# Optimization experiments

Hardware: AMD Instinct MI355X
Metric: run time of the kernel (lower is better)

## Reference

```python
import jax, jax.numpy as jnp
import numpy as np

N_NODES = 100000
N_EDGES = 1600000
IN_C, HID, N_CLS = 128, 128, 40


def setup_inputs() -> dict:
    key = jax.random.key(0)
    ks = jax.random.split(key, 8)
    x = jax.random.normal(ks[0], (N_NODES, IN_C), dtype=jnp.float32)
    edge_index = jax.random.randint(ks[1], (2, N_EDGES), 0, N_NODES, dtype=jnp.int64)
    s1 = 1.0 / np.sqrt(IN_C)
    s2 = 1.0 / np.sqrt(HID)
    return {
        "x": x,
        "edge_index": edge_index,
        "Wl1": jax.random.normal(ks[2], (IN_C, HID), dtype=jnp.float32) * s1,
        "Wr1": jax.random.normal(ks[3], (IN_C, HID), dtype=jnp.float32) * s1,
        "b1": jnp.zeros((HID,), dtype=jnp.float32),
        "Wl2": jax.random.normal(ks[4], (HID, N_CLS), dtype=jnp.float32) * s2,
        "Wr2": jax.random.normal(ks[5], (HID, N_CLS), dtype=jnp.float32) * s2,
        "b2": jnp.zeros((N_CLS,), dtype=jnp.float32),
    }


def _sage_conv(x, src, dst, Wl, Wr, b):
    # mean-aggregate neighbor features at destination nodes
    n = x.shape[0]
    agg = jax.ops.segment_sum(x[src], dst, num_segments=n)           # [N, C]
    cnt = jax.ops.segment_sum(jnp.ones((src.shape[0],), x.dtype), dst, num_segments=n)
    mean = agg / jnp.maximum(cnt, 1.0)[:, None]
    return mean @ Wl + x @ Wr + b


def reference(x, edge_index, Wl1, Wr1, b1, Wl2, Wr2, b2):
    src, dst = edge_index[0], edge_index[1]
    h = jax.nn.relu(_sage_conv(x, src, dst, Wl1, Wr1, b1))
    return _sage_conv(h, src, dst, Wl2, Wr2, b2)
```

## Files before the change

kernel.cpp:

```cpp
#include <hip/hip_runtime.h>

#define C_IN 128
#define N_CLS 40
#define ZB   40

#define NPB   256
#define MAXNB 512
#define CAP   6144
#define BCSTR 16
#define BINB  8192

typedef __attribute__((ext_vector_type(8))) short bf16x8;
typedef __attribute__((ext_vector_type(4))) float f32x4;
typedef __attribute__((ext_vector_type(2))) float f32x2;

__device__ __forceinline__ ushort f2b(float f) {
  union { float f; unsigned u; } v; v.f = f;
  unsigned r = v.u + 0x7FFF + ((v.u >> 16) & 1);
  return (ushort)(r >> 16);
}
__device__ __forceinline__ unsigned packbf(float lo, float hi) {
  return (unsigned)f2b(lo) | ((unsigned)f2b(hi) << 16);
}
__device__ __forceinline__ void acc2(float& fa, float& fb, unsigned u) {
  union { unsigned u; float f; } lo, hi;
  lo.u = u << 16; hi.u = u & 0xFFFF0000u;
  fa += lo.f; fb += hi.f;
}

#if __has_builtin(__builtin_amdgcn_cvt_pk_f32_fp8) && __has_builtin(__builtin_amdgcn_cvt_pk_fp8_f32)
#define HW_FP8 1
#else
#define HW_FP8 0
#endif

__device__ __forceinline__ float f8dec1(unsigned b) {
  unsigned E = (b >> 3) & 15, M = b & 7;
  if (E) {
    union { unsigned u; float f; } v;
    v.u = ((b & 0x80u) << 24) | ((E + 120u) << 23) | (M << 20);
    return v.f;
  }
  float m = (float)(int)M * 0.001953125f;
  return (b & 0x80u) ? -m : m;
}
__device__ __forceinline__ unsigned f8enc1(float x) {
  union { float f; unsigned u; } v; v.f = x;
  unsigned s = (v.u >> 31) << 7;
  float ax = fabsf(x);
  if (ax < 9.765625e-4f) return s;
  if (ax < 0.015625f) {
    int M = (int)rintf(ax * 512.0f);
    return (M >= 8) ? (s | 0x08u) : (s | (unsigned)M);
  }
  if (ax > 448.0f) return s | 0x7Eu;
  unsigned au = v.u & 0x7FFFFFFFu;
  unsigned r = au + 0x7FFFFu + ((au >> 20) & 1);
  int e = (int)(r >> 23) - 127;
  unsigned M = (r >> 20) & 7;
  if (e > 8) return s | 0x7Eu;
  return s | ((unsigned)(e + 7) << 3) | M;
}
__device__ __forceinline__ void accf8x4(float* a, unsigned u) {
#if HW_FP8
  f32x2 lo = __builtin_amdgcn_cvt_pk_f32_fp8((int)u, false);
  f32x2 hi = __builtin_amdgcn_cvt_pk_f32_fp8((int)u, true);
  a[0] += lo[0]; a[1] += lo[1]; a[2] += hi[0]; a[3] += hi[1];
#else
  a[0] += f8dec1(u & 0xFF); a[1] += f8dec1((u >> 8) & 0xFF);
  a[2] += f8dec1((u >> 16) & 0xFF); a[3] += f8dec1(u >> 24);
#endif
}
__device__ __forceinline__ unsigned packf8x4(float x0, float x1, float x2, float x3) {
#if HW_FP8
  int p = 0;
  p = __builtin_amdgcn_cvt_pk_fp8_f32(x0, x1, p, false);
  p = __builtin_amdgcn_cvt_pk_fp8_f32(x2, x3, p, true);
  return (unsigned)p;
#else
  return f8enc1(x0) | (f8enc1(x1) << 8) | (f8enc1(x2) << 16) | (f8enc1(x3) << 24);
#endif
}
__device__ __forceinline__ unsigned char f8enc_byte(float x) {
#if HW_FP8
  return (unsigned char)(__builtin_amdgcn_cvt_pk_fp8_f32(x, x, 0, false) & 0xFF);
#else
  return (unsigned char)f8enc1(x);
#endif
}

__global__ __launch_bounds__(256) void bin_cvt_kernel(
    const int* __restrict__ src, const int* __restrict__ dst,
    int* __restrict__ bcur, unsigned* __restrict__ staged, int E, int NB, int nbin,
    const float* __restrict__ xin, ushort* __restrict__ xb,
    unsigned char* __restrict__ xf8, long n8)
{
  __shared__ unsigned sw[BINB];
  __shared__ ushort  sb[BINB];
  __shared__ int cnt[MAXNB];
  __shared__ int base[MAXNB];
  const int tid = threadIdx.x;
  if (blockIdx.x >= nbin) {
    long i = ((long)(blockIdx.x - nbin) * 256 + tid);
    if (i < n8) {
      const float4 a = *reinterpret_cast<const float4*>(xin + i * 8);
      const float4 b = *reinterpret_cast<const float4*>(xin + i * 8 + 4);
      uint4 o;
      o.x = packbf(a.x, a.y);
      o.y = packbf(a.z, a.w);
      o.z = packbf(b.x, b.y);
      o.w = packbf(b.z, b.w);
      *reinterpret_cast<uint4*>(xb + i * 8) = o;
      uint2 p;
      p.x = packf8x4(a.x, a.y, a.z, a.w);
      p.y = packf8x4(b.x, b.y, b.z, b.w);
      *reinterpret_cast<uint2*>(xf8 + i * 8) = p;
    }
    return;
  }
  for (int i = tid; i < NB; i += 256) cnt[i] = 0;
  __syncthreads();
  const int e0 = blockIdx.x * BINB;
  const int nE = min(BINB, E - e0);
  for (int k = tid; k < nE; k += 256) {
    int d = dst[e0 + k];
    int s = src[e0 + k];
    int b = d >> 8;
    sw[k] = (unsigned)s | ((unsigned)(d & 255) << 20);
    sb[k] = (ushort)b;
    atomicAdd(&cnt[b], 1);
  }
  __syncthreads();
  for (int i = tid; i < NB; i += 256) {
    int c = cnt[i];
    base[i] = (c > 0) ? atomicAdd(&bcur[i * BCSTR], c) : 0;
    cnt[i] = 0;
  }
  __syncthreads();
  for (int k = tid; k < nE; k += 256) {
    int b = sb[k];
    int pos = base[b] + atomicAdd(&cnt[b], 1);
    if (pos < CAP)
      staged[(size_t)b * CAP + pos] = sw[k];
  }
}

__global__ __launch_bounds__(256) void csr_kernel(
    const unsigned* __restrict__ staged, const int* __restrict__ bcur,
    int* __restrict__ row_ptr, int* __restrict__ deg, int* __restrict__ csr_src, int N)
{
  __shared__ unsigned st[CAP];
  __shared__ int dcnt[NPB];
  __shared__ int cur[NPB];
  __shared__ int wsum[4];
  __shared__ int rb_s;
  const int b = blockIdx.x, tid = threadIdx.x;
  const int cb = min(bcur[b * BCSTR], CAP);
  for (int i = tid; i < cb; i += 256) st[i] = staged[(size_t)b * CAP + i];
  int part = 0;
  for (int i = tid; i < b; i += 256) part += min(bcur[i * BCSTR], CAP);
  if (tid == 0) rb_s = 0;
  dcnt[tid] = 0;
  __syncthreads();
  #pragma unroll
  for (int off = 32; off > 0; off >>= 1) part += __shfl_down(part, off);
  if ((tid & 63) == 0 && part != 0) atomicAdd(&rb_s, part);
  for (int i = tid; i < cb; i += 256) atomicAdd(&dcnt[st[i] >> 20], 1);
  __syncthreads();
  const int rb = rb_s;
  int d = dcnt[tid];
  const int lane = tid & 63, w = tid >> 6;
  int inc = d;
  #pragma unroll
  for (int off = 1; off < 64; off <<= 1) {
    int v = __shfl_up(inc, off);
    if (lane >= off) inc += v;
  }
  if (lane == 63) wsum[w] = inc;
  __syncthreads();
  int wo = 0;
  for (int i = 0; i < w; ++i) wo += wsum[i];
  const int excl = wo + inc - d;
  cur[tid] = excl;
  const int node = b * NPB + tid;
  if (node < N) { row_ptr[node] = rb + excl; deg[node] = d; }
  __syncthreads();
  for (int i = tid; i < cb; i += 256) {
    unsigned wv = st[i];
    int p = atomicAdd(&cur[wv >> 20], 1);
    csr_src[rb + p] = (int)(wv & 0xFFFFF);
  }
}

__global__ __launch_bounds__(256) void agg1_kernel(
    const unsigned char* __restrict__ xf8, const ushort* __restrict__ xb,
    const int* __restrict__ csr_src, const int* __restrict__ row_ptr,
    const int* __restrict__ deg, ushort* __restrict__ mean, int N)
{
  int t = blockIdx.x * 256 + threadIdx.x;
  int n = t >> 3;
  if (n >= N) return;
  int q = t & 7;
  int base = row_ptr[n];
  int d = deg[n];
  float a[16];
  #pragma unroll
  for (int i = 0; i < 16; ++i) a[i] = 0.f;
  if (d > 8) {
    const unsigned char* fq = xf8 + q * 16;
    int j = 0;
    for (; j + 4 <= d; j += 4) {
      int s0 = csr_src[base + j + 0];
      int s1 = csr_src[base + j + 1];
      int s2 = csr_src[base + j + 2];
      int s3 = csr_src[base + j + 3];
      uint4 v0 = *reinterpret_cast<const uint4*>(fq + (size_t)s0 * C_IN);
      uint4 v1 = *reinterpret_cast<const uint4*>(fq + (size_t)s1 * C_IN);
      uint4 v2 = *reinterpret_cast<const uint4*>(fq + (size_t)s2 * C_IN);
      uint4 v3 = *reinterpret_cast<const uint4*>(fq + (size_t)s3 * C_IN);
      accf8x4(a+0, v0.x); accf8x4(a+4, v0.y); accf8x4(a+8, v0.z); accf8x4(a+12, v0.w);
      accf8x4(a+0, v1.x); accf8x4(a+4, v1.y); accf8x4(a+8, v1.z); accf8x4(a+12, v1.w);
      accf8x4(a+0, v2.x); accf8x4(a+4, v2.y); accf8x4(a+8, v2.z); accf8x4(a+12, v2.w);
      accf8x4(a+0, v3.x); accf8x4(a+4, v3.y); accf8x4(a+8, v3.z); accf8x4(a+12, v3.w);
    }
    for (; j < d; ++j) {
      int s = csr_src[base + j];
      uint4 v = *reinterpret_cast<const uint4*>(fq + (size_t)s * C_IN);
      accf8x4(a+0, v.x); accf8x4(a+4, v.y); accf8x4(a+8, v.z); accf8x4(a+12, v.w);
    }
  } else {
    const ushort* fq = xb + q * 16;
    for (int j = 0; j < d; ++j) {
      int s = csr_src[base + j];
      uint4 w0 = *reinterpret_cast<const uint4*>(fq + (size_t)s * C_IN);
      uint4 w1 = *reinterpret_cast<const uint4*>(fq + (size_t)s * C_IN + 8);
      acc2(a[0],a[1],w0.x); acc2(a[2],a[3],w0.y); acc2(a[4],a[5],w0.z); acc2(a[6],a[7],w0.w);
      acc2(a[8],a[9],w1.x); acc2(a[10],a[11],w1.y); acc2(a[12],a[13],w1.z); acc2(a[14],a[15],w1.w);
    }
  }
  float inv = (d > 0) ? (1.0f / (float)d) : 0.0f;
  uint4 o0, o1;
  o0.x = packbf(a[0]*inv, a[1]*inv);  o0.y = packbf(a[2]*inv, a[3]*inv);
  o0.z = packbf(a[4]*inv, a[5]*inv);  o0.w = packbf(a[6]*inv, a[7]*inv);
  o1.x = packbf(a[8]*inv, a[9]*inv);  o1.y = packbf(a[10]*inv, a[11]*inv);
  o1.z = packbf(a[12]*inv, a[13]*inv); o1.w = packbf(a[14]*inv, a[15]*inv);
  uint4* mp = reinterpret_cast<uint4*>(mean + (size_t)n * C_IN + q * 16);
  mp[0] = o0;
  mp[1] = o1;
}

__global__ __launch_bounds__(256) void layer1_mfma(
    const ushort* __restrict__ xb, const ushort* __restrict__ mb,
    const float* __restrict__ Wr, const float* __restrict__ Wl,
    const float* __restrict__ bias, ushort* __restrict__ h, int N, int ntiles)
{
  __shared__ ushort sB[8 * 8 * 64 * 8];
  const int tid = threadIdx.x;
  for (int idx = tid; idx < 8 * 8 * 64; idx += 256) {
    int l  = idx & 63;
    int cg = (idx >> 6) & 7;
    int ks = idx >> 9;
    int c  = cg * 16 + (l & 15);
    int kb = ks * 32 + 8 * (l >> 4);
    ushort* p = &sB[idx * 8];
    #pragma unroll
    for (int j = 0; j < 8; ++j) {
      int k = kb + j;
      float w = (k < C_IN) ? Wr[k * C_IN + c] : Wl[(k - C_IN) * C_IN + c];
      p[j] = f2b(w);
    }
  }
  __syncthreads();
  const int w = tid >> 6, l = tid & 63;
  const int rfrag = l & 15, kg = l >> 4;
  for (int tile = blockIdx.x; tile < ntiles; tile += gridDim.x) {
    int n0 = tile * 128 + w * 32;
    int rc0 = n0 + rfrag;      rc0 = (rc0 < N) ? rc0 : (N - 1);
    int rc1 = n0 + 16 + rfrag; rc1 = (rc1 < N) ? rc1 : (N - 1);
    f32x4 acc[2][8] = {};
    #pragma unroll
    for (int ks = 0; ks < 8; ++ks) {
      int kb = ks * 32 + kg * 8;
      const ushort* Asrc = (kb < C_IN) ? (xb + kb) : (mb + (kb - C_IN));
      bf16x8 a0 = *reinterpret_cast<const bf16x8*>(Asrc + (size_t)rc0 * C_IN);
      bf16x8 a1 = *reinterpret_cast<const bf16x8*>(Asrc + (size_t)rc1 * C_IN);
      #pragma unroll
      for (int cg = 0; cg < 8; ++cg) {
        bf16x8 b = *reinterpret_cast<const bf16x8*>(&sB[((ks * 8 + cg) * 64 + l) * 8]);
        acc[0][cg] = __builtin_amdgcn_mfma_f32_16x16x32_bf16(a0, b, acc[0][cg], 0, 0, 0);
        acc[1][cg] = __builtin_amdgcn_mfma_f32_16x16x32_bf16(a1, b, acc[1][cg], 0, 0, 0);
      }
    }
    const int rowoff = (l >> 4) * 4, colbase = l & 15;
    #pragma unroll
    for (int f = 0; f < 2; ++f) {
      #pragma unroll
      for (int cg = 0; cg < 8; ++cg) {
        int c = cg * 16 + colbase;
        float bc = bias[c];
        #pragma unroll
        for (int r = 0; r < 4; ++r) {
          int row = n0 + f * 16 + rowoff + r;
          if (row < N) {
            float v = fmaxf(acc[f][cg][r] + bc, 0.0f);
            h[(size_t)row * C_IN + c] = f2b(v);
          }
        }
      }
    }
  }
}

__global__ __launch_bounds__(256) void gemm2_dual(
    const ushort* __restrict__ hb,
    const float* __restrict__ Wl, const float* __restrict__ Wr,
    unsigned char* __restrict__ z, float* __restrict__ out, int N, int ntiles)
{
  __shared__ ushort sBl[4 * 3 * 64 * 8];
  __shared__ ushort sBr[4 * 3 * 64 * 8];
  const int tid = threadIdx.x;
  for (int idx = tid; idx < 4 * 3 * 64; idx += 256) {
    int l  = idx & 63;
    int cg = (idx >> 6) % 3;
    int ks = idx / (3 * 64);
    int c  = cg * 16 + (l & 15);
    int kb = ks * 32 + 8 * (l >> 4);
    ushort* pl = &sBl[idx * 8];
    ushort* pr = &sBr[idx * 8];
    #pragma unroll
    for (int j = 0; j < 8; ++j) {
      int k = kb + j;
      float wl = 0.0f, wr = 0.0f;
      if (c < N_CLS) { wl = Wl[k * N_CLS + c]; wr = Wr[k * N_CLS + c]; }
      pl[j] = f2b(wl);
      pr[j] = f2b(wr);
    }
  }
  __syncthreads();
  const int w = tid >> 6, l = tid & 63;
  const int rfrag = l & 15, kg = l >> 4;
  for (int tile = blockIdx.x; tile < ntiles; tile += gridDim.x) {
    int n0 = tile * 128 + w * 32;
    int rc0 = n0 + rfrag;      rc0 = (rc0 < N) ? rc0 : (N - 1);
    int rc1 = n0 + 16 + rfrag; rc1 = (rc1 < N) ? rc1 : (N - 1);
    f32x4 az[2][3] = {};
    f32x4 ay[2][3] = {};
    #pragma unroll
    for (int ks = 0; ks < 4; ++ks) {
      int kb = ks * 32 + kg * 8;
      bf16x8 a0 = *reinterpret_cast<const bf16x8*>(hb + (size_t)rc0 * C_IN + kb);
      bf16x8 a1 = *reinterpret_cast<const bf16x8*>(hb + (size_t)rc1 * C_IN + kb);
      #pragma unroll
      for (int cg = 0; cg < 3; ++cg) {
        bf16x8 bl = *reinterpret_cast<const bf16x8*>(&sBl[((ks * 3 + cg) * 64 + l) * 8]);
        bf16x8 br = *reinterpret_cast<const bf16x8*>(&sBr[((ks * 3 + cg) * 64 + l) * 8]);
        az[0][cg] = __builtin_amdgcn_mfma_f32_16x16x32_bf16(a0, bl, az[0][cg], 0, 0, 0);
        az[1][cg] = __builtin_amdgcn_mfma_f32_16x16x32_bf16(a1, bl, az[1][cg], 0, 0, 0);
        ay[0][cg] = __builtin_amdgcn_mfma_f32_16x16x32_bf16(a0, br, ay[0][cg], 0, 0, 0);
        ay[1][cg] = __builtin_amdgcn_mfma_f32_16x16x32_bf16(a1, br, ay[1][cg], 0, 0, 0);
      }
    }
    const int rowoff = (l >> 4) * 4, colbase = l & 15;
    #pragma unroll
    for (int f = 0; f < 2; ++f) {
      #pragma unroll
      for (int cg = 0; cg < 3; ++cg) {
        int c = cg * 16 + colbase;
        if (c < N_CLS) {
          #pragma unroll
          for (int r = 0; r < 4; ++r) {
            int row = n0 + f * 16 + rowoff + r;
            if (row < N) {
              z[(size_t)row * ZB + c] = f8enc_byte(az[f][cg][r]);
              out[(size_t)row * N_CLS + c] = ay[f][cg][r];
            }
          }
        }
      }
    }
  }
}

__global__ __launch_bounds__(256) void agg2z_kernel(
    const unsigned char* __restrict__ z, const int* __restrict__ csr_src,
    const int* __restrict__ row_ptr, const int* __restrict__ deg,
    const float* __restrict__ b2, float* __restrict__ out, int N)
{
  unsigned w = blockIdx.x * 256 + threadIdx.x;
  unsigned n = w / 5u;
  if (n >= (unsigned)N) return;
  unsigned q = w - n * 5u;
  const unsigned char* zq = z + q * 8;
  int base = row_ptr[n];
  int d = deg[n];
  float a[8];
  #pragma unroll
  for (int i = 0; i < 8; ++i) a[i] = 0.f;
  int j = 0;
  for (; j + 4 <= d; j += 4) {
    int s0 = csr_src[base + j + 0];
    int s1 = csr_src[base + j + 1];
    int s2 = csr_src[base + j + 2];
    int s3 = csr_src[base + j + 3];
    uint2 v0 = *reinterpret_cast<const uint2*>(zq + (size_t)s0 * ZB);
    uint2 v1 = *reinterpret_cast<const uint2*>(zq + (size_t)s1 * ZB);
    uint2 v2 = *reinterpret_cast<const uint2*>(zq + (size_t)s2 * ZB);
    uint2 v3 = *reinterpret_cast<const uint2*>(zq + (size_t)s3 * ZB);
    accf8x4(a+0, v0.x); accf8x4(a+4, v0.y);
    accf8x4(a+0, v1.x); accf8x4(a+4, v1.y);
    accf8x4(a+0, v2.x); accf8x4(a+4, v2.y);
    accf8x4(a+0, v3.x); accf8x4(a+4, v3.y);
  }
  for (; j < d; ++j) {
    int s = csr_src[base + j];
    uint2 v = *reinterpret_cast<const uint2*>(zq + (size_t)s * ZB);
    accf8x4(a+0, v.x); accf8x4(a+4, v.y);
  }
  float inv = (d > 0) ? (1.0f / (float)d) : 0.0f;
  float* op = out + (size_t)n * N_CLS + q * 8;
  const float4 bA = *reinterpret_cast<const float4*>(b2 + q * 8);
  const float4 bB = *reinterpret_cast<const float4*>(b2 + q * 8 + 4);
  float4 y0 = *reinterpret_cast<const float4*>(op);
  float4 y1 = *reinterpret_cast<const float4*>(op + 4);
  y0.x += a[0] * inv + bA.x; y0.y += a[1] * inv + bA.y;
  y0.z += a[2] * inv + bA.z; y0.w += a[3] * inv + bA.w;
  y1.x += a[4] * inv + bB.x; y1.y += a[5] * inv + bB.y;
  y1.z += a[6] * inv + bB.z; y1.w += a[7] * inv + bB.w;
  *reinterpret_cast<float4*>(op) = y0;
  *reinterpret_cast<float4*>(op + 4) = y1;
}

extern "C" void kernel_launch(void* const* d_in, const int* in_sizes, int n_in,
                              void* d_out, int out_size, void* d_ws, size_t ws_size,
                              hipStream_t stream)
{
  const float* x   = (const float*)d_in[0];
  const int*   ei  = (const int*)d_in[1];
  const float* Wl1 = (const float*)d_in[2];
  const float* Wr1 = (const float*)d_in[3];
  const float* b1  = (const float*)d_in[4];
  const float* Wl2 = (const float*)d_in[5];
  const float* Wr2 = (const float*)d_in[6];
  const float* b2  = (const float*)d_in[7];
  float* out = (float*)d_out;

  const int N = in_sizes[0] / C_IN;
  const int E = in_sizes[1] / 2;
  const int* src = ei;
  const int* dst = ei + E;
  const int NB = (N + NPB - 1) / NPB;

  size_t Np = ((size_t)N + 255) & ~(size_t)255;
  size_t Ep = ((size_t)E + 255) & ~(size_t)255;
  int* wsi     = (int*)d_ws;
  int* bcur    = wsi;
  int* row_ptr = wsi + (size_t)MAXNB * BCSTR;
  int* deg     = row_ptr + Np;
  int* csr_src = deg + Np;
  unsigned* staged = (unsigned*)(csr_src + Ep);
  unsigned char* zb = (unsigned char*)staged;
  ushort* xb    = (ushort*)(staged + (size_t)MAXNB * CAP);
  ushort* meanb = xb + (size_t)N * C_IN;
  ushort* hb    = meanb + (size_t)N * C_IN;
  unsigned char* xf8 = (unsigned char*)(hb + (size_t)N * C_IN);

  hipMemsetAsync(bcur, 0, (size_t)MAXNB * BCSTR * sizeof(int), stream);

  const int nbin = (E + BINB - 1) / BINB;
  long n8 = (long)N * C_IN / 8;
  const int ncvt = (int)((n8 + 255) / 256);
  bin_cvt_kernel<<<nbin + ncvt, 256, 0, stream>>>(src, dst, bcur, staged, E, NB, nbin,
                                                  x, xb, xf8, n8);

  csr_kernel<<<NB, 256, 0, stream>>>(staged, bcur, row_ptr, deg, csr_src, N);

  const int ntiles = (N + 127) / 128;

  agg1_kernel<<<(N * 8 + 255) / 256, 256, 0, stream>>>(xf8, xb, csr_src, row_ptr, deg, meanb, N);
  layer1_mfma<<<512, 256, 0, stream>>>(xb, meanb, Wr1, Wl1, b1, hb, N, ntiles);

  gemm2_dual<<<512, 256, 0, stream>>>(hb, Wl2, Wr2, zb, out, N, ntiles);
  agg2z_kernel<<<(N * 5 + 255) / 256, 256, 0, stream>>>(zb, csr_src, row_ptr, deg, b2, out, N);
}
```

Before: 170.8 us.

## Transform-then-aggregate layer 1 and fuse CSR build with dense GEMM

Layer 1 is reordered so x is first multiplied by Wr and Wl, giving u = x@Wr + b and v = x@Wl. Neighbours of v are then mean-aggregated, and relu is applied to the sum with u inside the aggregation kernel. The dense GEMM now runs in the same launch as the CSR build, in extra blocks, because it does not depend on the graph. This removes one kernel launch and the separate mean buffer pass, and lets the GEMM overlap with CSR construction. In exchange, v is written in both fp8 and bf16 with scalar per-element stores, the xb buffer is overwritten in place, and the union shared-memory layout at 512 threads may reduce occupancy.

Measured after the change: 203.9 us. 1.19x slower.

```diff
diff --git a/kernel.cpp b/kernel.cpp
--- a/kernel.cpp
+++ b/kernel.cpp
@@ -26,6 +26,11 @@
   union { unsigned u; float f; } lo, hi;
   lo.u = u << 16; hi.u = u & 0xFFFF0000u;
   fa += lo.f; fb += hi.f;
+}
+__device__ __forceinline__ unsigned relu2add(float m0, float m1, unsigned uu) {
+  union { unsigned u; float f; } lo, hi;
+  lo.u = uu << 16; hi.u = uu & 0xFFFF0000u;
+  return packbf(fmaxf(m0 + lo.f, 0.0f), fmaxf(m1 + hi.f, 0.0f));
 }
 
 #if __has_builtin(__builtin_amdgcn_cvt_pk_f32_fp8) && __has_builtin(__builtin_amdgcn_cvt_pk_fp8_f32)
@@ -71,16 +76,6 @@
   a[2] += f8dec1((u >> 16) & 0xFF); a[3] += f8dec1(u >> 24);
 #endif
 }
-__device__ __forceinline__ unsigned packf8x4(float x0, float x1, float x2, float x3) {
-#if HW_FP8
-  int p = 0;
-  p = __builtin_amdgcn_cvt_pk_fp8_f32(x0, x1, p, false);
-  p = __builtin_amdgcn_cvt_pk_fp8_f32(x2, x3, p, true);
-  return (unsigned)p;
-#else
-  return f8enc1(x0) | (f8enc1(x1) << 8) | (f8enc1(x2) << 16) | (f8enc1(x3) << 24);
-#endif
-}
 __device__ __forceinline__ unsigned char f8enc_byte(float x) {
 #if HW_FP8
   return (unsigned char)(__builtin_amdgcn_cvt_pk_fp8_f32(x, x, 0, false) & 0xFF);
@@ -92,8 +87,7 @@
 __global__ __launch_bounds__(256) void bin_cvt_kernel(
     const int* __restrict__ src, const int* __restrict__ dst,
     int* __restrict__ bcur, unsigned* __restrict__ staged, int E, int NB, int nbin,
-    const float* __restrict__ xin, ushort* __restrict__ xb,
-    unsigned char* __restrict__ xf8, long n8)
+    const float* __restrict__ xin, ushort* __restrict__ xb, long n8)
 {
   __shared__ unsigned sw[BINB];
   __shared__ ushort  sb[BINB];
@@ -111,10 +105,6 @@
       o.z = packbf(b.x, b.y);
       o.w = packbf(b.z, b.w);
       *reinterpret_cast<uint4*>(xb + i * 8) = o;
-      uint2 p;
-      p.x = packf8x4(a.x, a.y, a.z, a.w);
-      p.y = packf8x4(b.x, b.y, b.z, b.w);
-      *reinterpret_cast<uint2*>(xf8 + i * 8) = p;
     }
     return;
   }
@@ -145,57 +135,127 @@
   }
 }
 
-__global__ __launch_bounds__(256) void csr_kernel(
+union SharedCG {
+  struct { unsigned st[CAP]; int dcnt[NPB]; int cur[NPB]; int wsum[4]; int rb_s; } c;
+  struct { ushort bu[4 * 8 * 64 * 8]; ushort bv[4 * 8 * 64 * 8]; } g;
+};
+
+__global__ __launch_bounds__(512) void csr_gemm1_kernel(
     const unsigned* __restrict__ staged, const int* __restrict__ bcur,
-    int* __restrict__ row_ptr, int* __restrict__ deg, int* __restrict__ csr_src, int N)
-{
-  __shared__ unsigned st[CAP];
-  __shared__ int dcnt[NPB];
-  __shared__ int cur[NPB];
-  __shared__ int wsum[4];
-  __shared__ int rb_s;
-  const int b = blockIdx.x, tid = threadIdx.x;
-  const int cb = min(bcur[b * BCSTR], CAP);
-  for (int i = tid; i < cb; i += 256) st[i] = staged[(size_t)b * CAP + i];
-  int part = 0;
-  for (int i = tid; i < b; i += 256) part += min(bcur[i * BCSTR], CAP);
-  if (tid == 0) rb_s = 0;
-  dcnt[tid] = 0;
+    int* __restrict__ row_ptr, int* __restrict__ deg, int* __restrict__ csr_src,
+    int N, int NB, int ntiles, int ngem,
+    ushort* __restrict__ xb,
+    const float* __restrict__ Wr, const float* __restrict__ Wl,
+    const float* __restrict__ bias,
+    ushort* __restrict__ u, unsigned char* __restrict__ vf8)
+{
+  __shared__ SharedCG sh;
+  const int tid = threadIdx.x;
+  if (blockIdx.x < NB) {
+    const int b = blockIdx.x;
+    const int cb = min(bcur[b * BCSTR], CAP);
+    for (int i = tid; i < cb; i += 512) sh.c.st[i] = staged[(size_t)b * CAP + i];
+    int part = 0;
+    for (int i = tid; i < b; i += 512) part += min(bcur[i * BCSTR], CAP);
+    if (tid == 0) sh.c.rb_s = 0;
+    if (tid < 256) sh.c.dcnt[tid] = 0;
+    __syncthreads();
+    #pragma unroll
+    for (int off = 32; off > 0; off >>= 1) part += __shfl_down(part, off);
+    if ((tid & 63) == 0 && part != 0) atomicAdd(&sh.c.rb_s, part);
+    for (int i = tid; i < cb; i += 512) atomicAdd(&sh.c.dcnt[sh.c.st[i] >> 20], 1);
+    __syncthreads();
+    const int rb = sh.c.rb_s;
+    int d = 0, excl = 0;
+    if (tid < 256) {
+      d = sh.c.dcnt[tid];
+      const int lane = tid & 63, w = tid >> 6;
+      int inc = d;
+      #pragma unroll
+      for (int off = 1; off < 64; off <<= 1) {
+        int v = __shfl_up(inc, off);
+        if (lane >= off) inc += v;
+      }
+      if (lane == 63) sh.c.wsum[w] = inc;
+      excl = inc - d;
+    }
+    __syncthreads();
+    if (tid < 256) {
+      int wo = 0;
+      for (int i = 0; i < (tid >> 6); ++i) wo += sh.c.wsum[i];
+      excl += wo;
+      sh.c.cur[tid] = excl;
+      const int node = b * NPB + tid;
+      if (node < N) { row_ptr[node] = rb + excl; deg[node] = d; }
+    }
+    __syncthreads();
+    for (int i = tid; i < cb; i += 512) {
+      unsigned wv = sh.c.st[i];
+      int p = atomicAdd(&sh.c.cur[wv >> 20], 1);
+      csr_src[rb + p] = (int)(wv & 0xFFFFF);
+    }
+    return;
+  }
+  for (int idx = tid; idx < 4 * 8 * 64; idx += 512) {
+    int l  = idx & 63;
+    int cg = (idx >> 6) & 7;
+    int ks = idx >> 9;
+    int c  = cg * 16 + (l & 15);
+    int kb = ks * 32 + 8 * (l >> 4);
+    ushort* pu = &sh.g.bu[idx * 8];
+    ushort* pv = &sh.g.bv[idx * 8];
+    #pragma unroll
+    for (int j = 0; j < 8; ++j) {
+      int k = kb + j;
+      pu[j] = f2b(Wr[k * C_IN + c]);
+      pv[j] = f2b(Wl[k * C_IN + c]);
+    }
+  }
   __syncthreads();
-  #pragma unroll
-  for (int off = 32; off > 0; off >>= 1) part += __shfl_down(part, off);
-  if ((tid & 63) == 0 && part != 0) atomicAdd(&rb_s, part);
-  for (int i = tid; i < cb; i += 256) atomicAdd(&dcnt[st[i] >> 20], 1);
-  __syncthreads();
-  const int rb = rb_s;
-  int d = dcnt[tid];
-  const int lane = tid & 63, w = tid >> 6;
-  int inc = d;
-  #pragma unroll
-  for (int off = 1; off < 64; off <<= 1) {
-    int v = __shfl_up(inc, off);
-    if (lane >= off) inc += v;
-  }
-  if (lane == 63) wsum[w] = inc;
-  __syncthreads();
-  int wo = 0;
-  for (int i = 0; i < w; ++i) wo += wsum[i];
-  const int excl = wo + inc - d;
-  cur[tid] = excl;
-  const int node = b * NPB + tid;
-  if (node < N) { row_ptr[node] = rb + excl; deg[node] = d; }
-  __syncthreads();
-  for (int i = tid; i < cb; i += 256) {
-    unsigned wv = st[i];
-    int p = atomicAdd(&cur[wv >> 20], 1);
-    csr_src[rb + p] = (int)(wv & 0xFFFFF);
-  }
-}
-
-__global__ __launch_bounds__(256) void agg1_kernel(
-    const unsigned char* __restrict__ xf8, const ushort* __restrict__ xb,
-    const int* __restrict__ csr_src, const int* __restrict__ row_ptr,
-    const int* __restrict__ deg, ushort* __restrict__ mean, int N)
+  const int wv = tid >> 6, l = tid & 63;
+  const int kg = l >> 4;
+  for (int tile = blockIdx.x - NB; tile < ntiles; tile += ngem) {
+    const int n0 = tile * 128 + wv * 16;
+    int rc = n0 + (l & 15); rc = (rc < N) ? rc : (N - 1);
+    f32x4 au[8] = {};
+    f32x4 av[8] = {};
+    #pragma unroll
+    for (int ks = 0; ks < 4; ++ks) {
+      int kb = ks * 32 + kg * 8;
+      bf16x8 a = *reinterpret_cast<const bf16x8*>(xb + (size_t)rc * C_IN + kb);
+      #pragma unroll
+      for (int cg = 0; cg < 8; ++cg) {
+        bf16x8 bu = *reinterpret_cast<const bf16x8*>(&sh.g.bu[((ks * 8 + cg) * 64 + l) * 8]);
+        bf16x8 bv = *reinterpret_cast<const bf16x8*>(&sh.g.bv[((ks * 8 + cg) * 64 + l) * 8]);
+        au[cg] = __builtin_amdgcn_mfma_f32_16x16x32_bf16(a, bu, au[cg], 0, 0, 0);
+        av[cg] = __builtin_amdgcn_mfma_f32_16x16x32_bf16(a, bv, av[cg], 0, 0, 0);
+      }
+    }
+    const int rowoff = (l >> 4) * 4, colbase = l & 15;
+    #pragma unroll
+    for (int cg = 0; cg < 8; ++cg) {
+      int c = cg * 16 + colbase;
+      float bc = bias[c];
+      #pragma unroll
+      for (int r = 0; r < 4; ++r) {
+        int row = n0 + rowoff + r;
+        if (row < N) {
+          float uu = au[cg][r] + bc;
+          float vvv = av[cg][r];
+          u[(size_t)row * C_IN + c] = f2b(uu);
+          vf8[(size_t)row * C_IN + c] = f8enc_byte(vvv);
+          xb[(size_t)row * C_IN + c] = f2b(vvv);
+        }
+      }
+    }
+  }
+}
+
+__global__ __launch_bounds__(256) void agg1v_kernel(
+    const unsigned char* __restrict__ vf8, const ushort* __restrict__ vb,
+    const ushort* __restrict__ u, const int* __restrict__ csr_src,
+    const int* __restrict__ row_ptr, const int* __restrict__ deg,
+    ushort* __restrict__ h, int N)
 {
   int t = blockIdx.x * 256 + threadIdx.x;
   int n = t >> 3;
@@ -207,7 +267,7 @@
   #pragma unroll
   for (int i = 0; i < 16; ++i) a[i] = 0.f;
   if (d > 8) {
-    const unsigned char* fq = xf8 + q * 16;
+    const unsigned char* fq = vf8 + q * 16;
     int j = 0;
     for (; j + 4 <= d; j += 4) {
       int s0 = csr_src[base + j + 0];
@@ -229,7 +289,7 @@
       accf8x4(a+0, v.x); accf8x4(a+4, v.y); accf8x4(a+8, v.z); accf8x4(a+12, v.w);
     }
   } else {
-    const ushort* fq = xb + q * 16;
+    const ushort* fq = vb + q * 16;
     for (int j = 0; j < d; ++j) {
       int s = csr_src[base + j];
       uint4 w0 = *reinterpret_cast<const uint4*>(fq + (size_t)s * C_IN);
@@ -239,76 +299,21 @@
     }
   }
   float inv = (d > 0) ? (1.0f / (float)d) : 0.0f;
+  const ushort* up = u + (size_t)n * C_IN + q * 16;
+  uint4 u0 = *reinterpret_cast<const uint4*>(up);
+  uint4 u1 = *reinterpret_cast<const uint4*>(up + 8);
   uint4 o0, o1;
-  o0.x = packbf(a[0]*inv, a[1]*inv);  o0.y = packbf(a[2]*inv, a[3]*inv);
-  o0.z = packbf(a[4]*inv, a[5]*inv);  o0.w = packbf(a[6]*inv, a[7]*inv);
-  o1.x = packbf(a[8]*inv, a[9]*inv);  o1.y = packbf(a[10]*inv, a[11]*inv);
-  o1.z = packbf(a[12]*inv, a[13]*inv); o1.w = packbf(a[14]*inv, a[15]*inv);
-  uint4* mp = reinterpret_cast<uint4*>(mean + (size_t)n * C_IN + q * 16);
-  mp[0] = o0;
-  mp[1] = o1;
-}
-
-__global__ __launch_bounds__(256) void layer1_mfma(
-    const ushort* __restrict__ xb, const ushort* __restrict__ mb,
-    const float* __restrict__ Wr, const float* __restrict__ Wl,
-    const float* __restrict__ bias, ushort* __restrict__ h, int N, int ntiles)
-{
-  __shared__ ushort sB[8 * 8 * 64 * 8];
-  const int tid = threadIdx.x;
-  for (int idx = tid; idx < 8 * 8 * 64; idx += 256) {
-    int l  = idx & 63;
-    int cg = (idx >> 6) & 7;
-    int ks = idx >> 9;
-    int c  = cg * 16 + (l & 15);
-    int kb = ks * 32 + 8 * (l >> 4);
-    ushort* p = &sB[idx * 8];
-    #pragma unroll
-    for (int j = 0; j < 8; ++j) {
-      int k = kb + j;
-      float w = (k < C_IN) ? Wr[k * C_IN + c] : Wl[(k - C_IN) * C_IN + c];
-      p[j] = f2b(w);
-    }
-  }
-  __syncthreads();
-  const int w = tid >> 6, l = tid & 63;
-  const int rfrag = l & 15, kg = l >> 4;
-  for (int tile = blockIdx.x; tile < ntiles; tile += gridDim.x) {
-    int n0 = tile * 128 + w * 32;
-    int rc0 = n0 + rfrag;      rc0 = (rc0 < N) ? rc0 : (N - 1);
-    int rc1 = n0 + 16 + rfrag; rc1 = (rc1 < N) ? rc1 : (N - 1);
-    f32x4 acc[2][8] = {};
-    #pragma unroll
-    for (int ks = 0; ks < 8; ++ks) {
-      int kb = ks * 32 + kg * 8;
-      const ushort* Asrc = (kb < C_IN) ? (xb + kb) : (mb + (kb - C_IN));
-      bf16x8 a0 = *reinterpret_cast<const bf16x8*>(Asrc + (size_t)rc0 * C_IN);
-      bf16x8 a1 = *reinterpret_cast<const bf16x8*>(Asrc + (size_t)rc1 * C_IN);
-      #pragma unroll
-      for (int cg = 0; cg < 8; ++cg) {
-        bf16x8 b = *reinterpret_cast<const bf16x8*>(&sB[((ks * 8 + cg) * 64 + l) * 8]);
-        acc[0][cg] = __builtin_amdgcn_mfma_f32_16x16x32_bf16(a0, b, acc[0][cg], 0, 0, 0);
-        acc[1][cg] = __builtin_amdgcn_mfma_f32_16x16x32_bf16(a1, b, acc[1][cg], 0, 0, 0);
-      }
-    }
-    const int rowoff = (l >> 4) * 4, colbase = l & 15;
-    #pragma unroll
-    for (int f = 0; f < 2; ++f) {
-      #pragma unroll
-      for (int cg = 0; cg < 8; ++cg) {
-        int c = cg * 16 + colbase;
-        float bc = bias[c];
-        #pragma unroll
-        for (int r = 0; r < 4; ++r) {
-          int row = n0 + f * 16 + rowoff + r;
-          if (row < N) {
-            float v = fmaxf(acc[f][cg][r] + bc, 0.0f);
-            h[(size_t)row * C_IN + c] = f2b(v);
-          }
-        }
-      }
-    }
-  }
+  o0.x = relu2add(a[0]*inv,  a[1]*inv,  u0.x);
+  o0.y = relu2add(a[2]*inv,  a[3]*inv,  u0.y);
+  o0.z = relu2add(a[4]*inv,  a[5]*inv,  u0.z);
+  o0.w = relu2add(a[6]*inv,  a[7]*inv,  u0.w);
+  o1.x = relu2add(a[8]*inv,  a[9]*inv,  u1.x);
+  o1.y = relu2add(a[10]*inv, a[11]*inv, u1.y);
+  o1.z = relu2add(a[12]*inv, a[13]*inv, u1.z);
+  o1.w = relu2add(a[14]*inv, a[15]*inv, u1.w);
+  uint4* hp = reinterpret_cast<uint4*>(h + (size_t)n * C_IN + q * 16);
+  hp[0] = o0;
+  hp[1] = o1;
 }
 
 __global__ __launch_bounds__(256) void gemm2_dual(
@@ -460,9 +465,9 @@
   unsigned* staged = (unsigned*)(csr_src + Ep);
   unsigned char* zb = (unsigned char*)staged;
   ushort* xb    = (ushort*)(staged + (size_t)MAXNB * CAP);
-  ushort* meanb = xb + (size_t)N * C_IN;
-  ushort* hb    = meanb + (size_t)N * C_IN;
-  unsigned char* xf8 = (unsigned char*)(hb + (size_t)N * C_IN);
+  ushort* ub    = xb + (size_t)N * C_IN;
+  ushort* hb    = ub + (size_t)N * C_IN;
+  unsigned char* vf8 = (unsigned char*)(hb + (size_t)N * C_IN);
 
   hipMemsetAsync(bcur, 0, (size_t)MAXNB * BCSTR * sizeof(int), stream);
 
@@ -470,14 +475,16 @@
   long n8 = (long)N * C_IN / 8;
   const int ncvt = (int)((n8 + 255) / 256);
   bin_cvt_kernel<<<nbin + ncvt, 256, 0, stream>>>(src, dst, bcur, staged, E, NB, nbin,
-                                                  x, xb, xf8, n8);
-
-  csr_kernel<<<NB, 256, 0, stream>>>(staged, bcur, row_ptr, deg, csr_src, N);
+                                                  x, xb, n8);
 
   const int ntiles = (N + 127) / 128;
-
-  agg1_kernel<<<(N * 8 + 255) / 256, 256, 0, stream>>>(xf8, xb, csr_src, row_ptr, deg, meanb, N);
-  layer1_mfma<<<512, 256, 0, stream>>>(xb, meanb, Wr1, Wl1, b1, hb, N, ntiles);
+  const int ngem = 512;
+
+  csr_gemm1_kernel<<<NB + ngem, 512, 0, stream>>>(staged, bcur, row_ptr, deg, csr_src,
+                                                  N, NB, ntiles, ngem,
+                                                  xb, Wr1, Wl1, b1, ub, vf8);
+
+  agg1v_kernel<<<(N * 8 + 255) / 256, 256, 0, stream>>>(vf8, xb, ub, csr_src, row_ptr, deg, hb, N);
 
   gemm2_dual<<<512, 256, 0, stream>>>(hb, Wl2, Wr2, zb, out, N, ntiles);
   agg2z_kernel<<<(N * 5 + 255) / 256, 256, 0, stream>>>(zb, csr_src, row_ptr, deg, b2, out, N);
```

## Split layer-1 GEMM to overlap x@Wr with neighbor aggregation in one launch

Applied to the files above, without the earlier changes.

Layer 1 is split into two half-K GEMMs. The x@Wr+b part runs as extra blocks appended to the aggregation kernel, so the compute-bound MFMA work can overlap with the gather-bound aggregation, and it writes a bf16 intermediate u. The second kernel loads u as the accumulator, adds mean@Wl and applies ReLU. This adds an extra N×128 bf16 write and read of u, an extra rounding of the partial sum to bf16, and shared memory in the aggregation blocks, which may lower their occupancy.

Result: slower. 196.2 us (+14.9%).

```diff
diff --git a/kernel.cpp b/kernel.cpp
--- a/kernel.cpp
+++ b/kernel.cpp
@@ -18,6 +18,10 @@
   union { float f; unsigned u; } v; v.f = f;
   unsigned r = v.u + 0x7FFF + ((v.u >> 16) & 1);
   return (ushort)(r >> 16);
+}
+__device__ __forceinline__ float b2f(ushort u) {
+  union { unsigned u; float f; } v; v.u = ((unsigned)u) << 16;
+  return v.f;
 }
 __device__ __forceinline__ unsigned packbf(float lo, float hi) {
   return (unsigned)f2b(lo) | ((unsigned)f2b(hi) << 16);
@@ -192,12 +196,64 @@
   }
 }
 
-__global__ __launch_bounds__(256) void agg1_kernel(
+__global__ __launch_bounds__(256) void agg1_ugemm_kernel(
     const unsigned char* __restrict__ xf8, const ushort* __restrict__ xb,
     const int* __restrict__ csr_src, const int* __restrict__ row_ptr,
-    const int* __restrict__ deg, ushort* __restrict__ mean, int N)
-{
-  int t = blockIdx.x * 256 + threadIdx.x;
+    const int* __restrict__ deg, ushort* __restrict__ mean, int N, int nagg,
+    const float* __restrict__ Wr, const float* __restrict__ bias,
+    ushort* __restrict__ u, int ntiles, int ngem)
+{
+  __shared__ ushort sB[4 * 8 * 64 * 8];
+  const int tid = threadIdx.x;
+  if (blockIdx.x >= nagg) {
+    for (int idx = tid; idx < 4 * 8 * 64; idx += 256) {
+      int l  = idx & 63;
+      int cg = (idx >> 6) & 7;
+      int ks = idx >> 9;
+      int c  = cg * 16 + (l & 15);
+      int kb = ks * 32 + 8 * (l >> 4);
+      ushort* p = &sB[idx * 8];
+      #pragma unroll
+      for (int j = 0; j < 8; ++j) p[j] = f2b(Wr[(kb + j) * C_IN + c]);
+    }
+    __syncthreads();
+    const int w = tid >> 6, l = tid & 63;
+    const int kg = l >> 4;
+    for (int tile = blockIdx.x - nagg; tile < ntiles; tile += ngem) {
+      int n0 = tile * 128 + w * 32;
+      int rc0 = n0 + (l & 15);      rc0 = (rc0 < N) ? rc0 : (N - 1);
+      int rc1 = n0 + 16 + (l & 15); rc1 = (rc1 < N) ? rc1 : (N - 1);
+      f32x4 acc[2][8] = {};
+      #pragma unroll
+      for (int ks = 0; ks < 4; ++ks) {
+        int kb = ks * 32 + kg * 8;
+        bf16x8 a0 = *reinterpret_cast<const bf16x8*>(xb + (size_t)rc0 * C_IN + kb);
+        bf16x8 a1 = *reinterpret_cast<const bf16x8*>(xb + (size_t)rc1 * C_IN + kb);
+        #pragma unroll
+        for (int cg = 0; cg < 8; ++cg) {
+          bf16x8 b = *reinterpret_cast<const bf16x8*>(&sB[((ks * 8 + cg) * 64 + l) * 8]);
+          acc[0][cg] = __builtin_amdgcn_mfma_f32_16x16x32_bf16(a0, b, acc[0][cg], 0, 0, 0);
+          acc[1][cg] = __builtin_amdgcn_mfma_f32_16x16x32_bf16(a1, b, acc[1][cg], 0, 0, 0);
+        }
+      }
+      const int rowoff = (l >> 4) * 4, colbase = l & 15;
+      #pragma unroll
+      for (int f = 0; f < 2; ++f) {
+        #pragma unroll
+        for (int cg = 0; cg < 8; ++cg) {
+          int c = cg * 16 + colbase;
+          float bc = bias[c];
+          #pragma unroll
+          for (int r = 0; r < 4; ++r) {
+            int row = n0 + f * 16 + rowoff + r;
+            if (row < N) u[(size_t)row * C_IN + c] = f2b(acc[f][cg][r] + bc);
+          }
+        }
+      }
+    }
+    return;
+  }
+  int t = blockIdx.x * 256 + tid;
   int n = t >> 3;
   if (n >= N) return;
   int q = t & 7;
@@ -249,14 +305,13 @@
   mp[1] = o1;
 }
 
-__global__ __launch_bounds__(256) void layer1_mfma(
-    const ushort* __restrict__ xb, const ushort* __restrict__ mb,
-    const float* __restrict__ Wr, const float* __restrict__ Wl,
-    const float* __restrict__ bias, ushort* __restrict__ h, int N, int ntiles)
-{
-  __shared__ ushort sB[8 * 8 * 64 * 8];
+__global__ __launch_bounds__(256) void layer1b_mfma(
+    const ushort* __restrict__ mb, const ushort* __restrict__ u,
+    const float* __restrict__ Wl, ushort* __restrict__ h, int N, int ntiles)
+{
+  __shared__ ushort sB[4 * 8 * 64 * 8];
   const int tid = threadIdx.x;
-  for (int idx = tid; idx < 8 * 8 * 64; idx += 256) {
+  for (int idx = tid; idx < 4 * 8 * 64; idx += 256) {
     int l  = idx & 63;
     int cg = (idx >> 6) & 7;
     int ks = idx >> 9;
@@ -264,26 +319,35 @@
     int kb = ks * 32 + 8 * (l >> 4);
     ushort* p = &sB[idx * 8];
     #pragma unroll
-    for (int j = 0; j < 8; ++j) {
-      int k = kb + j;
-      float w = (k < C_IN) ? Wr[k * C_IN + c] : Wl[(k - C_IN) * C_IN + c];
-      p[j] = f2b(w);
-    }
+    for (int j = 0; j < 8; ++j) p[j] = f2b(Wl[(kb + j) * C_IN + c]);
   }
   __syncthreads();
   const int w = tid >> 6, l = tid & 63;
-  const int rfrag = l & 15, kg = l >> 4;
+  const int kg = l >> 4;
+  const int rowoff = (l >> 4) * 4, colbase = l & 15;
   for (int tile = blockIdx.x; tile < ntiles; tile += gridDim.x) {
     int n0 = tile * 128 + w * 32;
-    int rc0 = n0 + rfrag;      rc0 = (rc0 < N) ? rc0 : (N - 1);
-    int rc1 = n0 + 16 + rfrag; rc1 = (rc1 < N) ? rc1 : (N - 1);
-    f32x4 acc[2][8] = {};
-    #pragma unroll
-    for (int ks = 0; ks < 8; ++ks) {
+    int rc0 = n0 + (l & 15);      rc0 = (rc0 < N) ? rc0 : (N - 1);
+    int rc1 = n0 + 16 + (l & 15); rc1 = (rc1 < N) ? rc1 : (N - 1);
+    f32x4 acc[2][8];
+    #pragma unroll
+    for (int f = 0; f < 2; ++f) {
+      #pragma unroll
+      for (int cg = 0; cg < 8; ++cg) {
+        int c = cg * 16 + colbase;
+        #pragma unroll
+        for (int r = 0; r < 4; ++r) {
+          int row = n0 + f * 16 + rowoff + r;
+          row = (row < N) ? row : (N - 1);
+          acc[f][cg][r] = b2f(u[(size_t)row * C_IN + c]);
+        }
+      }
+    }
+    #pragma unroll
+    for (int ks = 0; ks < 4; ++ks) {
       int kb = ks * 32 + kg * 8;
-      const ushort* Asrc = (kb < C_IN) ? (xb + kb) : (mb + (kb - C_IN));
-      bf16x8 a0 = *reinterpret_cast<const bf16x8*>(Asrc + (size_t)rc0 * C_IN);
-      bf16x8 a1 = *reinterpret_cast<const bf16x8*>(Asrc + (size_t)rc1 * C_IN);
+      bf16x8 a0 = *reinterpret_cast<const bf16x8*>(mb + (size_t)rc0 * C_IN + kb);
+      bf16x8 a1 = *reinterpret_cast<const bf16x8*>(mb + (size_t)rc1 * C_IN + kb);
       #pragma unroll
       for (int cg = 0; cg < 8; ++cg) {
         bf16x8 b = *reinterpret_cast<const bf16x8*>(&sB[((ks * 8 + cg) * 64 + l) * 8]);
@@ -291,20 +355,16 @@
         acc[1][cg] = __builtin_amdgcn_mfma_f32_16x16x32_bf16(a1, b, acc[1][cg], 0, 0, 0);
       }
     }
-    const int rowoff = (l >> 4) * 4, colbase = l & 15;
     #pragma unroll
     for (int f = 0; f < 2; ++f) {
       #pragma unroll
       for (int cg = 0; cg < 8; ++cg) {
         int c = cg * 16 + colbase;
-        float bc = bias[c];
         #pragma unroll
         for (int r = 0; r < 4; ++r) {
           int row = n0 + f * 16 + rowoff + r;
-          if (row < N) {
-            float v = fmaxf(acc[f][cg][r] + bc, 0.0f);
-            h[(size_t)row * C_IN + c] = f2b(v);
-          }
+          if (row < N)
+            h[(size_t)row * C_IN + c] = f2b(fmaxf(acc[f][cg][r], 0.0f));
         }
       }
     }
@@ -462,7 +522,8 @@
   ushort* xb    = (ushort*)(staged + (size_t)MAXNB * CAP);
   ushort* meanb = xb + (size_t)N * C_IN;
   ushort* hb    = meanb + (size_t)N * C_IN;
-  unsigned char* xf8 = (unsigned char*)(hb + (size_t)N * C_IN);
+  ushort* ub    = hb + (size_t)N * C_IN;
+  unsigned char* xf8 = (unsigned char*)(ub + (size_t)N * C_IN);
 
   hipMemsetAsync(bcur, 0, (size_t)MAXNB * BCSTR * sizeof(int), stream);
 
@@ -475,9 +536,13 @@
   csr_kernel<<<NB, 256, 0, stream>>>(staged, bcur, row_ptr, deg, csr_src, N);
 
   const int ntiles = (N + 127) / 128;
-
-  agg1_kernel<<<(N * 8 + 255) / 256, 256, 0, stream>>>(xf8, xb, csr_src, row_ptr, deg, meanb, N);
-  layer1_mfma<<<512, 256, 0, stream>>>(xb, meanb, Wr1, Wl1, b1, hb, N, ntiles);
+  const int nagg = (N * 8 + 255) / 256;
+  const int ngem = 512;
+
+  agg1_ugemm_kernel<<<nagg + ngem, 256, 0, stream>>>(xf8, xb, csr_src, row_ptr, deg,
+                                                     meanb, N, nagg,
+                                                     Wr1, b1, ub, ntiles, ngem);
+  layer1b_mfma<<<512, 256, 0, stream>>>(meanb, ub, Wl1, hb, N, ntiles);
 
   gemm2_dual<<<512, 256, 0, stream>>>(hb, Wl2, Wr2, zb, out, N, ntiles);
   agg2z_kernel<<<(N * 5 + 255) / 256, 256, 0, stream>>>(zb, csr_src, row_ptr, deg, b2, out, N);
```
